# Performance work log

Measured on AMD Instinct MI355X. Metric: run time of the kernel, lower is better.

Reference implementation:

```python
import jax, jax.numpy as jnp
import numpy as np

S, B, L = 64, 32, 64
VS, VT = 32000, 32000
D_EMB, H_ENC, H_DEC = 300, 512, 1024


def _lstm_cell(x, h, c, w_ih, w_hh, b):
    # PyTorch gate order: i, f, g, o
    g = x @ w_ih.T + h @ w_hh.T + b
    i, f, gg, o = jnp.split(g, 4, axis=1)
    c2 = jax.nn.sigmoid(f) * c + jax.nn.sigmoid(i) * jnp.tanh(gg)
    h2 = jax.nn.sigmoid(o) * jnp.tanh(c2)
    return h2, c2


def _lstm_dir(emb, w_ih, w_hh, b, reverse):
    h0 = jnp.zeros((emb.shape[1], H_ENC), emb.dtype)
    def step(carry, x):
        h, c = carry
        h, c = _lstm_cell(x, h, c, w_ih, w_hh, b)
        return (h, c), h
    (hT, cT), ys = jax.lax.scan(step, (h0, h0), emb, reverse=reverse)
    return ys, hT, cT


def setup_inputs() -> dict:
    key = jax.random.key(0)
    ks = jax.random.split(key, 20)
    r = lambda k, shape: (jax.random.normal(k, shape, jnp.float32) * 0.02)
    inp = {
        "eemb": r(ks[0], (VS, D_EMB)),
        "enc_w_ih_f": r(ks[1], (4 * H_ENC, D_EMB)),
        "enc_w_hh_f": r(ks[2], (4 * H_ENC, H_ENC)),
        "enc_b_f": r(ks[3], (4 * H_ENC,)),  # = b_ih + b_hh (summed, identical math)
        "enc_w_ih_b": r(ks[4], (4 * H_ENC, D_EMB)),
        "enc_w_hh_b": r(ks[5], (4 * H_ENC, H_ENC)),
        "enc_b_b": r(ks[6], (4 * H_ENC,)),
        "attn_wi": r(ks[7], (H_DEC, H_DEC)),
        "attn_wo": r(ks[8], (H_DEC, 2 * H_DEC)),
        "dec_w_ih": r(ks[9], (4 * H_DEC, H_DEC + D_EMB)),
        "dec_w_hh": r(ks[10], (4 * H_DEC, H_DEC)),
        "dec_b": r(ks[11], (4 * H_DEC,)),
        "demb": r(ks[12], (VT, D_EMB)),
        "gen_w": r(ks[13], (VT, H_DEC)),
        "gen_b": r(ks[14], (VT,)),
        "input_src_batch": jax.random.randint(ks[15], (S, B), 0, VS),
        "input_trg_batch": jax.random.randint(ks[16], (L, B), 0, VT),
    }
    return inp


def reference(eemb, enc_w_ih_f, enc_w_hh_f, enc_b_f, enc_w_ih_b, enc_w_hh_b,
              enc_b_b, attn_wi, attn_wo, dec_w_ih, dec_w_hh, dec_b, demb,
              gen_w, gen_b, input_src_batch, input_trg_batch):
    emb = eemb[input_src_batch]  # [S,B,300]
    out_f, hf, cf = _lstm_dir(emb, enc_w_ih_f, enc_w_hh_f, enc_b_f, False)
    out_b, hb, cb = _lstm_dir(emb, enc_w_ih_b, enc_w_hh_b, enc_b_b, True)
    enc_out = jnp.concatenate([out_f, out_b], axis=2)  # [S,B,1024]
    bsz = emb.shape[1]
    # permute(1,2,0).view(B,1024): interleave fwd/bwd features
    hidden = jnp.stack([hf, hb], 0).transpose(1, 2, 0).reshape(bsz, H_DEC)
    context = jnp.stack([cf, cb], 0).transpose(1, 2, 0).reshape(bsz, H_DEC)

    trg_emb = demb[input_trg_batch[:-1]]  # [L-1,B,300]

    def dec_step(carry, e):
        h, c = carry
        semi = h @ attn_wi.T  # [B,1024]
        scores = jax.nn.softmax(jnp.sum(enc_out * semi[None], axis=2), axis=0)  # [S,B]
        s_tilde = jnp.sum(scores[:, :, None] * enc_out, axis=0)  # [B,1024]
        c_t = jnp.tanh(jnp.concatenate([s_tilde, h], axis=1) @ attn_wo.T)
        x = jnp.concatenate([c_t, e], axis=1)  # [B,1324]
        h, c = _lstm_cell(x, h, c, dec_w_ih, dec_w_hh, dec_b)
        out = jax.nn.log_softmax(h @ gen_w.T + gen_b, axis=1)  # [B,VT]
        return (h, c), out

    _, ys = jax.lax.scan(dec_step, (hidden, context), trg_emb)  # [L-1,B,VT]
    output = jnp.concatenate([jnp.zeros((1,) + ys.shape[1:], ys.dtype), ys], axis=0)
    return output
```

## Files before the change

kernel.cpp:

```cpp
#include <hip/hip_runtime.h>

typedef __attribute__((ext_vector_type(8))) short short8;
typedef __attribute__((ext_vector_type(4))) float f32x4;
typedef unsigned short u16;
typedef unsigned int u32;

static __device__ __forceinline__ float sigf(float x){ return 1.0f/(1.0f+expf(-x)); }

static __device__ __forceinline__ u16 f2b(float f){
    u32 u = __float_as_uint(f);
    u += 0x7FFFu + ((u>>16)&1u);
    return (u16)(u>>16);
}
static __device__ __forceinline__ float us2f(u16 s){ return __uint_as_float(((u32)s)<<16); }
static __device__ __forceinline__ float b2f_lo(u32 u){ return __uint_as_float(u<<16); }
static __device__ __forceinline__ float b2f_hi(u32 u){ return __uint_as_float(u & 0xffff0000u); }

static __device__ __forceinline__ void st_wt_u16(u16* p, u16 v) {
    asm volatile("global_store_short %0, %1, off sc1" :: "v"(p), "v"((u32)v) : "memory");
}
static __device__ __forceinline__ void st_wt_u32(u32* p, u32 v) {
    asm volatile("global_store_dword %0, %1, off sc1" :: "v"(p), "v"(v) : "memory");
}
static __device__ __forceinline__ u32 ld_cv(const u32* p){
    u32 v;
    asm volatile("global_load_dword %0, %1, off sc0 sc1\ns_waitcnt vmcnt(0)"
                 : "=v"(v) : "v"(p) : "memory");
    return v;
}

static __device__ __forceinline__ void hot_spin() {
    float x = 1.0f;
#pragma unroll
    for (int i = 0; i < 16; ++i) x = __builtin_fmaf(x, 1.0000001f, 1.0e-7f);
    asm volatile("" :: "v"(x));
}

static __device__ __forceinline__ void wait_publish(const u32* base, int n, u32 tgt, u32* rel) {
    if ((int)threadIdx.x < n) {
        const u32* p = base + (size_t)threadIdx.x*32;
        while (ld_cv(p) < tgt) hot_spin();
    }
    __syncthreads();
    if (threadIdx.x == 0) st_wt_u32(rel, tgt);
}
static __device__ __forceinline__ void wait_rel(const u32* rel, u32 tgt) {
    if (threadIdx.x == 0) {
        while (ld_cv(rel) < tgt) hot_spin();
    }
    __syncthreads();
}


__global__ __launch_bounds__(256) void k_zero(float* __restrict__ p, long n) {
    for (long i = (long)blockIdx.x*256 + threadIdx.x; i < n; i += (long)gridDim.x*256) p[i] = 0.0f;
}

__global__ __launch_bounds__(256) void k_wenc(const float* __restrict__ whh, u16* __restrict__ dst) {
    int i = blockIdx.x*256 + threadIdx.x;
    int n = i >> 9, k = i & 511;
    int j = n >> 2, q = n & 3;
    dst[i] = f2b(whh[(size_t)(q*512 + j)*512 + k]);
}

__global__ __launch_bounds__(256) void k_xw(const float* __restrict__ table,
                                            const int* __restrict__ idx,
                                            const float* __restrict__ W,
                                            int wstride, int koff,
                                            const float* __restrict__ bias,
                                            u16* __restrict__ outU, int N,
                                            int jmask, int jshift) {
    __shared__ float Xs[32][300];
    int m0 = blockIdx.y * 32;
    int j0 = blockIdx.x * 64;
    for (int i = threadIdx.x; i < 32*300; i += 256) {
        int r = i/300, c = i - r*300;
        Xs[r][c] = table[(size_t)idx[m0+r]*300 + c];
    }
    __syncthreads();
    int tx = threadIdx.x & 63, ty = threadIdx.x >> 6;
    int jj = j0 + tx;
    const float* wr = W + (size_t)jj*wstride + koff;
    float acc[8] = {0,0,0,0,0,0,0,0};
    for (int k = 0; k < 300; ++k) {
        float w = wr[k];
#pragma unroll
        for (int mi = 0; mi < 8; ++mi) acc[mi] += Xs[ty*8+mi][k] * w;
    }
    float bv = bias[jj];
    int col = ((jj & jmask) << 2) | (jj >> jshift);
#pragma unroll
    for (int mi = 0; mi < 8; ++mi)
        outU[(size_t)(m0 + ty*8 + mi)*N + col] = f2b(acc[mi] + bv);
}

__global__ __launch_bounds__(512, 1) void k_enc(
    const u16* __restrict__ Xf, const u16* __restrict__ Xb,
    const u16* __restrict__ WencB,
    u16* __restrict__ encBX, float* __restrict__ cfin,
    u32* __restrict__ sentE, u32* __restrict__ relE,
    const float* __restrict__ awi, const float* __restrict__ awo,
    const float* __restrict__ dwih, const float* __restrict__ dwhh,
    const float* __restrict__ genw,
    u16* __restrict__ awiTB, u16* __restrict__ awoB,
    u16* __restrict__ WdecB, u16* __restrict__ genw_b)
{
    __shared__ float SH[2304];
    const int tid = threadIdx.x;
    const int bid = blockIdx.x;

    if (bid >= 64) {
        long wid = (long)(bid-64)*512 + tid;
        {
            const float4* s4 = (const float4*)genw;
            ushort4* d4 = (ushort4*)genw_b;
            for (long i = wid; i < 8192000L; i += 98304L) {
                float4 v = s4[i]; ushort4 u;
                u.x=f2b(v.x); u.y=f2b(v.y); u.z=f2b(v.z); u.w=f2b(v.w);
                d4[i]=u;
            }
        }
        for (long i = wid; i < 8388608L; i += 98304L) {
            int n=(int)(i>>11), k=(int)(i&2047);
            int j=n>>2, q=n&3;
            float v=(k<1024)? dwih[(size_t)(q*1024+j)*1324+k]
                            : dwhh[(size_t)(q*1024+j)*1024+(k-1024)];
            WdecB[i]=f2b(v);
        }
        for (long i = wid; i < 1048576L; i += 98304L) {
            int kcol=(int)(i>>10), n=(int)(i&1023);
            awiTB[i]=f2b(awi[(size_t)n*1024+kcol]);
        }
        {
            const float4* s4=(const float4*)awo;
            ushort4* d4=(ushort4*)awoB;
            for (long i = wid; i < 524288L; i += 98304L) {
                float4 v=s4[i]; ushort4 u;
                u.x=f2b(v.x); u.y=f2b(v.y); u.z=f2b(v.z); u.w=f2b(v.w);
                d4[i]=u;
            }
        }
        return;
    }

    const int wv = tid >> 6, lane = tid & 63;
    const int gwave = bid*8 + wv;
    const int lr = lane & 15, lk8 = (lane >> 4)*8;
    const int b_l = lane & 15, jjq = lane >> 4;
    const int g0 = bid & 48;
    u32* relg = relE + (size_t)(g0 >> 4)*32;

    const int dir = gwave >> 8;
    const int mt = (gwave >> 7) & 1;
    const int nt = gwave & 127;
    const int m0 = mt*16, n0 = nt*16;
    const u16* Bw = WencB + (size_t)dir*1048576 + (size_t)(n0+lr)*512 + lk8;
    const u16* Xd = dir ? Xb : Xf;
    float* T = SH + wv*272;
    const int bb = m0 + b_l;
    const int j = nt*4 + jjq;

    short8 bw[16];
#pragma unroll
    for (int i = 0; i < 16; ++i) bw[i] = *(const short8*)(Bw + i*32);

    float creg = 0.f;
    for (int t = 0; t < 64; ++t) {
        if (t > 0) {
            if (bid == g0) wait_publish(sentE + (size_t)g0*32, 16, (u32)t, relg);
            else           wait_rel(relg, (u32)t);
        }
        const int rslot = (t==0) ? 0 : (dir ? (65-t) : t);
        const u16* Ah = encBX + (size_t)rslot*32768 + (size_t)(m0+lr)*1024 + dir*512 + lk8;
        short8 av[16];
#pragma unroll
        for (int i = 0; i < 16; ++i) av[i] = *(const short8*)(Ah + i*32);
        f32x4 acc = {0.f,0.f,0.f,0.f};
#pragma unroll
        for (int i = 0; i < 16; ++i)
            acc = __builtin_amdgcn_mfma_f32_16x16x32_bf16(av[i], bw[i], acc, 0, 0, 0);
        {
            const int rb = (lane>>4)*4;
#pragma unroll
            for (int r = 0; r < 4; ++r) T[(rb+r)*17 + (lane&15)] = acc[r];
        }
        __builtin_amdgcn_sched_barrier(0);
        const int s = dir ? (63-t) : t;
        ushort4 xr = *(const ushort4*)(Xd + (size_t)(s*32+bb)*2048 + n0 + jjq*4);
        float gi = T[b_l*17 + jjq*4 + 0] + us2f(xr.x);
        float gf = T[b_l*17 + jjq*4 + 1] + us2f(xr.y);
        float gg = T[b_l*17 + jjq*4 + 2] + us2f(xr.z);
        float go = T[b_l*17 + jjq*4 + 3] + us2f(xr.w);
        float c2 = sigf(gf)*creg + sigf(gi)*tanhf(gg);
        float h2 = sigf(go)*tanhf(c2);
        creg = c2;
        st_wt_u16(encBX + (size_t)(s+1)*32768 + (size_t)bb*1024 + dir*512 + j, f2b(h2));
        __syncthreads();
        if (tid == 0) st_wt_u32(sentE + (size_t)bid*32, (u32)(t+1));
    }
    cfin[dir*16384 + bb*512 + j] = creg;
}

__global__ __launch_bounds__(256) void k_mid(const u16* __restrict__ encBX,
                                             const u16* __restrict__ awiTB,
                                             const u16* __restrict__ awoB,
                                             u16* __restrict__ encPB,
                                             u16* __restrict__ EOAb,
                                             u16* __restrict__ Hd) {
    if (blockIdx.x < 128) {
        int gt = blockIdx.x*256 + threadIdx.x;
        int b = gt >> 10, jj2 = gt & 1023;
        int d = jj2 & 1, k = jj2 >> 1;
        Hd[(size_t)b*1024 + jj2] = encBX[(size_t)(d ? 1 : 64)*32768 + (size_t)b*1024 + d*512 + k];
        Hd[(size_t)64*32768 + gt] = 0;
    }
    const int wv = threadIdx.x >> 6, lane = threadIdx.x & 63;
    const int lr = lane & 15, lk8 = (lane >> 4)*8;
    const u16* Abase = encBX + 32768;
#pragma unroll
    for (int ii = 0; ii < 4; ++ii) {
        int id = (blockIdx.x*4 + wv)*4 + ii;
        int eoa = id >> 13;
        int id2 = id & 8191;
        int mt2 = id2 >> 6, nt2 = id2 & 63;
        int m0 = mt2*16, n0 = nt2*16;
        const u16* Ar = Abase + (size_t)(m0+lr)*1024 + lk8;
        const u16* Br = eoa ? (awoB + (size_t)(n0+lr)*2048 + lk8)
                            : (awiTB + (size_t)(n0+lr)*1024 + lk8);
        f32x4 acc = {0.f,0.f,0.f,0.f};
#pragma unroll 8
        for (int i = 0; i < 32; ++i) {
            short8 av = *(const short8*)(Ar + i*32);
            short8 bv = *(const short8*)(Br + i*32);
            acc = __builtin_amdgcn_mfma_f32_16x16x32_bf16(av, bv, acc, 0, 0, 0);
        }
        int col = n0 + (lane&15);
        int rb = m0 + (lane>>4)*4;
#pragma unroll
        for (int r = 0; r < 4; ++r) {
            int row = rb + r;
            if (eoa) {
                int b = row & 31, s = row >> 5;
                EOAb[((size_t)b*64 + s)*1024 + col] = f2b(acc[r]);
            } else {
                encPB[(size_t)row*1024 + col] = f2b(acc[r]);
            }
        }
    }
}

__global__ __launch_bounds__(512, 1) void k_dec(
    const u16* __restrict__ Xe,
    const u16* __restrict__ awoB, const u16* __restrict__ WdecB,
    const u16* __restrict__ encPB, const u16* __restrict__ EOAb,
    u16* __restrict__ Hd, u16* __restrict__ PEOb, u16* __restrict__ hAb,
    const float* __restrict__ cfin,
    u32* __restrict__ sentA, u32* __restrict__ sentH,
    u32* __restrict__ relA, u32* __restrict__ relH)
{
    __shared__ float SH[2592];
    __shared__ u32 CT[16512];
    const int tid = threadIdx.x;
    const int bid = blockIdx.x;
    const int wv = tid >> 6, lane = tid & 63;
    const int lr = lane & 15, lk8 = (lane >> 4)*8;
    const int b_l = lane & 15, jjq = lane >> 4;

    const int mt4 = wv & 1, kq4 = wv >> 1;
    const int m0d = mt4*16;
    const int bbd = m0d + b_l;
    const int jd = bid*4 + jjq;
    float cdec = cfin[(jd&1)*16384 + bbd*512 + (jd>>1)];

    short8 wp[16];
#pragma unroll
    for (int i = 0; i < 16; ++i)
        wp[i] = *(const short8*)(WdecB + (size_t)(bid*16+lr)*2048 + kq4*512 + lk8 + i*32);

    const bool isHA = (bid >= 32 && bid < 96);
    const int nth = bid - 32;
    const int mth = wv & 1, kqh = wv >> 1;
    short8 wh[8];
    if (isHA) {
#pragma unroll
        for (int i = 0; i < 8; ++i)
            wh[i] = *(const short8*)(awoB + (size_t)(nth*16+lr)*2048 + 1024 + kqh*256 + lk8 + i*32);
    }

    for (int t = 0; t < 63; ++t) {
        if (bid < 96) {
            if (t > 0) {
                if (bid == 0) wait_publish(sentH, 256, (u32)t, relH);
                else          wait_rel(relH, (u32)t);
            }
            if (bid < 32) {
                const int b = bid;
                float* hsh = SH; float* red = SH + 1024; float* sc = SH + 1536;
                {
                    u32 u = ((const u32*)Hd)[(size_t)t*16384 + b*512 + tid];
                    hsh[2*tid]   = b2f_lo(u);
                    hsh[2*tid+1] = b2f_hi(u);
                }
                __syncthreads();
                {
                    int s = tid >> 3, p = tid & 7;
                    const uint4* ep = (const uint4*)(encPB + (size_t)(s*32+b)*1024 + p*128);
                    const float* hk = hsh + p*128;
                    float a0=0,a1=0,a2=0,a3=0;
#pragma unroll 4
                    for (int q8 = 0; q8 < 16; ++q8) {
                        uint4 u = ep[q8];
                        a0 += b2f_lo(u.x)*hk[q8*8+0] + b2f_hi(u.x)*hk[q8*8+1];
                        a1 += b2f_lo(u.y)*hk[q8*8+2] + b2f_hi(u.y)*hk[q8*8+3];
                        a2 += b2f_lo(u.z)*hk[q8*8+4] + b2f_hi(u.z)*hk[q8*8+5];
                        a3 += b2f_lo(u.w)*hk[q8*8+6] + b2f_hi(u.w)*hk[q8*8+7];
                    }
                    red[tid] = (a0+a1)+(a2+a3);
                }
                __syncthreads();
                if (tid < 64) {
                    float v = 0;
#pragma unroll
                    for (int pp = 0; pp < 8; ++pp) v += red[tid*8+pp];
                    float m = v;
                    for (int off = 32; off; off >>= 1) m = fmaxf(m, __shfl_xor(m, off));
                    float e = expf(v - m);
                    float ss = e;
                    for (int off = 32; off; off >>= 1) ss += __shfl_xor(ss, off);
                    sc[tid] = e / ss;
                }
                __syncthreads();
                {
                    const u32* eo = (const u32*)EOAb + (size_t)b*32768 + tid;
                    float p0 = 0, p1 = 0;
#pragma unroll 8
                    for (int s = 0; s < 64; ++s) {
                        u32 u = eo[(size_t)s*512];
                        float w = sc[s];
                        p0 += w*b2f_lo(u); p1 += w*b2f_hi(u);
                    }
                    u32 pk = (u32)f2b(p0) | ((u32)f2b(p1) << 16);
                    st_wt_u32((u32*)PEOb + (size_t)t*16384 + b*512 + tid, pk);
                }
            } else {
                const u16* Ah = Hd + (size_t)t*32768 + (size_t)(mth*16+lr)*1024 + kqh*256 + lk8;
                short8 av[8];
#pragma unroll
                for (int i = 0; i < 8; ++i) av[i] = *(const short8*)(Ah + i*32);
                f32x4 acc = {0.f,0.f,0.f,0.f};
#pragma unroll
                for (int i = 0; i < 8; ++i)
                    acc = __builtin_amdgcn_mfma_f32_16x16x32_bf16(av[i], wh[i], acc, 0, 0, 0);
#pragma unroll
                for (int r = 0; r < 4; ++r) SH[wv*256 + lane*4 + r] = acc[r];
                __syncthreads();
                if (wv < 2) {
#pragma unroll
                    for (int r = 0; r < 4; ++r) {
                        float sum = SH[(wv+0)*256 + lane*4 + r] + SH[(wv+2)*256 + lane*4 + r]
                                  + SH[(wv+4)*256 + lane*4 + r] + SH[(wv+6)*256 + lane*4 + r];
                        int m = wv*16 + (lane>>4)*4 + r;
                        st_wt_u16(hAb + (size_t)t*32768 + (size_t)m*1024 + nth*16 + (lane&15),
                                  f2b(sum));
                    }
                }
            }
            __syncthreads();
            if (tid == 0) st_wt_u32(sentA + (size_t)bid*32, (u32)(t+1));
        }

        if (bid == 96) wait_publish(sentA, 96, (u32)(t+1), relA);
        else           wait_rel(relA, (u32)(t+1));
        {
            const u32* pe = (const u32*)PEOb + (size_t)t*16384;
            const u32* ha = (const u32*)hAb + (size_t)t*16384;
#pragma unroll
            for (int ii = 0; ii < 32; ++ii) {
                int idx = tid + ii*512;
                u32 up = pe[idx], uh = ha[idx];
                float c0 = tanhf(b2f_lo(up) + b2f_lo(uh));
                float c1 = tanhf(b2f_hi(up) + b2f_hi(uh));
                int b = idx >> 9, nu = idx & 511;
                CT[b*516 + nu] = (u32)f2b(c0) | ((u32)f2b(c1) << 16);
            }
            __syncthreads();

            short8 av[16];
            if (kq4 < 2) {
                const u32* ctrow = CT + (m0d+lr)*516 + kq4*256 + (lk8 >> 1);
#pragma unroll
                for (int i = 0; i < 16; ++i) av[i] = *(const short8*)(ctrow + i*16);
            } else {
                const u16* Ab = Hd + (size_t)t*32768 + (size_t)(m0d+lr)*1024 + (kq4-2)*512 + lk8;
#pragma unroll
                for (int i = 0; i < 16; ++i) av[i] = *(const short8*)(Ab + i*32);
            }
            f32x4 acc = {0.f,0.f,0.f,0.f};
#pragma unroll
            for (int i = 0; i < 16; ++i)
                acc = __builtin_amdgcn_mfma_f32_16x16x32_bf16(av[i], wp[i], acc, 0, 0, 0);
#pragma unroll
            for (int r = 0; r < 4; ++r) SH[wv*256 + lane*4 + r] = acc[r];
            __syncthreads();
            if (wv < 2) {
                float* T = SH + 2048 + wv*272;
#pragma unroll
                for (int r = 0; r < 4; ++r) {
                    float sum = SH[(wv+0)*256 + lane*4 + r] + SH[(wv+2)*256 + lane*4 + r]
                              + SH[(wv+4)*256 + lane*4 + r] + SH[(wv+6)*256 + lane*4 + r];
                    T[((lane>>4)*4 + r)*17 + (lane&15)] = sum;
                }
                __builtin_amdgcn_sched_barrier(0);
                ushort4 xr = *(const ushort4*)(Xe + (size_t)(t*32+bbd)*4096 + bid*16 + jjq*4);
                float gi = T[b_l*17 + jjq*4 + 0] + us2f(xr.x);
                float gf = T[b_l*17 + jjq*4 + 1] + us2f(xr.y);
                float gg = T[b_l*17 + jjq*4 + 2] + us2f(xr.z);
                float go = T[b_l*17 + jjq*4 + 3] + us2f(xr.w);
                float c2 = sigf(gf)*cdec + sigf(gi)*tanhf(gg);
                float h2 = sigf(go)*tanhf(c2);
                cdec = c2;
                st_wt_u16(Hd + (size_t)(t+1)*32768 + (size_t)bbd*1024 + jd, f2b(h2));
            }
            __syncthreads();
            if (tid == 0) st_wt_u32(sentH + (size_t)bid*32, (u32)(t+1));
        }
    }
}

__global__ __launch_bounds__(256) void k_gemm_gen(const short* __restrict__ A,
                                                  const short* __restrict__ B,
                                                  const float* __restrict__ genb,
                                                  float* __restrict__ out) {
    int wave = threadIdx.x >> 6;
    int lane = threadIdx.x & 63;
    int tile = blockIdx.x * 4 + wave;
    int mt = tile & 31;
    int nt = tile >> 5;
    int m0 = mt*64, n0 = nt*64;
    int lr = lane & 15;
    int lk = (lane >> 4)*8;
    f32x4 acc[4][4] = {};
    for (int k0 = 0; k0 < 1024; k0 += 32) {
        short8 a[4], bfr[4];
#pragma unroll
        for (int mi = 0; mi < 4; ++mi)
            a[mi] = *(const short8*)(A + (long)(m0 + mi*16 + lr)*1024 + k0 + lk);
#pragma unroll
        for (int ni = 0; ni < 4; ++ni)
            bfr[ni] = *(const short8*)(B + (long)(n0 + ni*16 + lr)*1024 + k0 + lk);
#pragma unroll
        for (int mi = 0; mi < 4; ++mi)
#pragma unroll
            for (int ni = 0; ni < 4; ++ni)
                acc[mi][ni] = __builtin_amdgcn_mfma_f32_16x16x32_bf16(a[mi], bfr[ni], acc[mi][ni], 0, 0, 0);
    }
    int dcol = lane & 15;
    int drow = (lane >> 4)*4;
#pragma unroll
    for (int mi = 0; mi < 4; ++mi) {
        int mbase = m0 + mi*16 + drow;
#pragma unroll
        for (int ni = 0; ni < 4; ++ni) {
            int n = n0 + ni*16 + dcol;
            float bv = genb[n];
            f32x4 v = acc[mi][ni];
#pragma unroll
            for (int r = 0; r < 4; ++r) {
                int m = mbase + r;
                if (m < 2016) out[(long)(m + 32)*32000 + n] = v[r] + bv;
            }
        }
    }
}

__global__ __launch_bounds__(256) void k_lsm(float* __restrict__ out) {
    long row = 32 + blockIdx.x;
    float* p = out + row*32000L;
    float4* p4 = (float4*)p;
    int tid = threadIdx.x;
    __shared__ float sm[4];
    __shared__ float ss[4];
    float m = -1e30f;
    for (int i = tid; i < 8000; i += 256) {
        float4 v = p4[i];
        m = fmaxf(m, fmaxf(fmaxf(v.x, v.y), fmaxf(v.z, v.w)));
    }
    for (int off = 32; off; off >>= 1) m = fmaxf(m, __shfl_xor(m, off));
    if ((tid & 63) == 0) sm[tid >> 6] = m;
    __syncthreads();
    m = fmaxf(fmaxf(sm[0], sm[1]), fmaxf(sm[2], sm[3]));
    float s = 0;
    for (int i = tid; i < 8000; i += 256) {
        float4 v = p4[i];
        s += expf(v.x - m) + expf(v.y - m) + expf(v.z - m) + expf(v.w - m);
    }
    for (int off = 32; off; off >>= 1) s += __shfl_xor(s, off);
    if ((tid & 63) == 0) ss[tid >> 6] = s;
    __syncthreads();
    s = ss[0] + ss[1] + ss[2] + ss[3];
    float lse = m + logf(s);
    for (int i = tid; i < 8000; i += 256) {
        float4 v = p4[i];
        v.x -= lse; v.y -= lse; v.z -= lse; v.w -= lse;
        p4[i] = v;
    }
}


extern "C" void kernel_launch(void* const* d_in, const int* in_sizes, int n_in,
                              void* d_out, int out_size, void* d_ws, size_t ws_size,
                              hipStream_t stream) {
    const float* eemb  = (const float*)d_in[0];
    const float* ewihf = (const float*)d_in[1];
    const float* ewhhf = (const float*)d_in[2];
    const float* ebf   = (const float*)d_in[3];
    const float* ewihb = (const float*)d_in[4];
    const float* ewhhb = (const float*)d_in[5];
    const float* ebb   = (const float*)d_in[6];
    const float* awi   = (const float*)d_in[7];
    const float* awo   = (const float*)d_in[8];
    const float* dwih  = (const float*)d_in[9];
    const float* dwhh  = (const float*)d_in[10];
    const float* db    = (const float*)d_in[11];
    const float* demb  = (const float*)d_in[12];
    const float* genw  = (const float*)d_in[13];
    const float* genb  = (const float*)d_in[14];
    const int* srci    = (const int*)d_in[15];
    const int* trgi    = (const int*)d_in[16];
    float* out = (float*)d_out;

    float* F = (float*)d_ws;
    u32* S       = (u32*)F;
    u32* sentE   = S;
    u32* sentA   = S + 2048;
    u32* sentH   = S + 5120;
    u32* relE    = S + 13312;
    u32* relA    = S + 13440;
    u32* relH    = S + 13472;
    float* cfin  = F + 16384;
    u16*   U     = (u16*)(F + 49152);

    u16* Xf_    = U;
    u16* Xb_    = U + 4194304u;
    u16* Xe_    = U + 8388608u;
    u16* WencB  = U + 16646144u;
    u16* awiTB  = U + 18743296u;
    u16* awoB   = U + 19791872u;
    u16* WdecB  = U + 21889024u;
    u16* genw_b = U + 30277632u;
    u16* encBX  = U + 63045632u;
    u16* Hd     = U + 65175552u;
    u16* PEOb   = U + 67305472u;
    u16* hAb    = U + 69369856u;
    u16* encPB  = U + 71434240u;
    u16* EOAb   = U + 73531392u;

    k_zero<<<64, 256, 0, stream>>>(F, 16384);
    k_zero<<<64, 256, 0, stream>>>((float*)encBX, 16384);
    k_zero<<<2048, 256, 0, stream>>>(out, 1024000L);

    k_xw<<<dim3(32, 64), 256, 0, stream>>>(eemb, srci, ewihf, 300, 0, ebf, Xf_, 2048, 511, 9);
    k_xw<<<dim3(32, 64), 256, 0, stream>>>(eemb, srci, ewihb, 300, 0, ebb, Xb_, 2048, 511, 9);
    k_xw<<<dim3(64, 63), 256, 0, stream>>>(demb, trgi, dwih, 1324, 1024, db, Xe_, 4096, 1023, 10);

    k_wenc<<<4096, 256, 0, stream>>>(ewhhf, WencB);
    k_wenc<<<4096, 256, 0, stream>>>(ewhhb, WencB + 1048576u);

    k_enc<<<256, 512, 0, stream>>>(Xf_, Xb_, WencB, encBX, cfin, sentE, relE,
                                   awi, awo, dwih, dwhh, genw,
                                   awiTB, awoB, WdecB, genw_b);
    k_mid<<<1024, 256, 0, stream>>>(encBX, awiTB, awoB, encPB, EOAb, Hd);

    k_dec<<<256, 512, 0, stream>>>(Xe_, awoB, WdecB, encPB, EOAb,
                                   Hd, PEOb, hAb, cfin,
                                   sentA, sentH, relA, relH);

    k_gemm_gen<<<4000, 256, 0, stream>>>((const short*)(Hd + 32768u), (const short*)genw_b, genb, out);
    k_lsm<<<2016, 256, 0, stream>>>(out);
}
```

Baseline: 2.995 ms.

## Use fast exp/tanh intrinsics, merge weight conversion, enlarge generator GEMM tiles

Result: faster. 2.633 ms (-12.1%).

```diff
diff --git a/kernel.cpp b/kernel.cpp
--- a/kernel.cpp
+++ b/kernel.cpp
@@ -5,7 +5,11 @@
 typedef unsigned short u16;
 typedef unsigned int u32;
 
-static __device__ __forceinline__ float sigf(float x){ return 1.0f/(1.0f+expf(-x)); }
+static __device__ __forceinline__ float sigf(float x){ return 1.0f/(1.0f+__expf(-x)); }
+static __device__ __forceinline__ float ftanh(float x){
+    float e = __expf(2.0f*x);
+    return 1.0f - 2.0f/(e + 1.0f);
+}
 
 static __device__ __forceinline__ u16 f2b(float f){
     u32 u = __float_as_uint(f);
@@ -56,11 +60,16 @@
     for (long i = (long)blockIdx.x*256 + threadIdx.x; i < n; i += (long)gridDim.x*256) p[i] = 0.0f;
 }
 
-__global__ __launch_bounds__(256) void k_wenc(const float* __restrict__ whh, u16* __restrict__ dst) {
-    int i = blockIdx.x*256 + threadIdx.x;
-    int n = i >> 9, k = i & 511;
+__global__ __launch_bounds__(256) void k_wenc2(const float* __restrict__ whhf,
+                                               const float* __restrict__ whhb,
+                                               u16* __restrict__ dst) {
+    long i = (long)blockIdx.x*256 + threadIdx.x;
+    int half = (int)(i >> 20);
+    int ii = (int)(i & 1048575);
+    int n = ii >> 9, k = ii & 511;
     int j = n >> 2, q = n & 3;
-    dst[i] = f2b(whh[(size_t)(q*512 + j)*512 + k]);
+    const float* w = half ? whhb : whhf;
+    dst[i] = f2b(w[(size_t)(q*512 + j)*512 + k]);
 }
 
 __global__ __launch_bounds__(256) void k_xw(const float* __restrict__ table,
@@ -191,8 +200,8 @@
         float gf = T[b_l*17 + jjq*4 + 1] + us2f(xr.y);
         float gg = T[b_l*17 + jjq*4 + 2] + us2f(xr.z);
         float go = T[b_l*17 + jjq*4 + 3] + us2f(xr.w);
-        float c2 = sigf(gf)*creg + sigf(gi)*tanhf(gg);
-        float h2 = sigf(go)*tanhf(c2);
+        float c2 = sigf(gf)*creg + sigf(gi)*ftanh(gg);
+        float h2 = sigf(go)*ftanh(c2);
         creg = c2;
         st_wt_u16(encBX + (size_t)(s+1)*32768 + (size_t)bb*1024 + dir*512 + j, f2b(h2));
         __syncthreads();
@@ -324,7 +333,7 @@
                     for (int pp = 0; pp < 8; ++pp) v += red[tid*8+pp];
                     float m = v;
                     for (int off = 32; off; off >>= 1) m = fmaxf(m, __shfl_xor(m, off));
-                    float e = expf(v - m);
+                    float e = __expf(v - m);
                     float ss = e;
                     for (int off = 32; off; off >>= 1) ss += __shfl_xor(ss, off);
                     sc[tid] = e / ss;
@@ -378,8 +387,8 @@
             for (int ii = 0; ii < 32; ++ii) {
                 int idx = tid + ii*512;
                 u32 up = pe[idx], uh = ha[idx];
-                float c0 = tanhf(b2f_lo(up) + b2f_lo(uh));
-                float c1 = tanhf(b2f_hi(up) + b2f_hi(uh));
+                float c0 = ftanh(b2f_lo(up) + b2f_lo(uh));
+                float c1 = ftanh(b2f_hi(up) + b2f_hi(uh));
                 int b = idx >> 9, nu = idx & 511;
                 CT[b*516 + nu] = (u32)f2b(c0) | ((u32)f2b(c1) << 16);
             }
@@ -416,8 +425,8 @@
                 float gf = T[b_l*17 + jjq*4 + 1] + us2f(xr.y);
                 float gg = T[b_l*17 + jjq*4 + 2] + us2f(xr.z);
                 float go = T[b_l*17 + jjq*4 + 3] + us2f(xr.w);
-                float c2 = sigf(gf)*cdec + sigf(gi)*tanhf(gg);
-                float h2 = sigf(go)*tanhf(c2);
+                float c2 = sigf(gf)*cdec + sigf(gi)*ftanh(gg);
+                float h2 = sigf(go)*ftanh(c2);
                 cdec = c2;
                 st_wt_u16(Hd + (size_t)(t+1)*32768 + (size_t)bbd*1024 + jd, f2b(h2));
             }
@@ -427,37 +436,36 @@
     }
 }
 
-__global__ __launch_bounds__(256) void k_gemm_gen(const short* __restrict__ A,
-                                                  const short* __restrict__ B,
-                                                  const float* __restrict__ genb,
-                                                  float* __restrict__ out) {
+__global__ __launch_bounds__(256, 1) void k_gemm_gen(const short* __restrict__ A,
+                                                     const short* __restrict__ B,
+                                                     const float* __restrict__ genb,
+                                                     float* __restrict__ out) {
     int wave = threadIdx.x >> 6;
     int lane = threadIdx.x & 63;
     int tile = blockIdx.x * 4 + wave;
-    int mt = tile & 31;
-    int nt = tile >> 5;
-    int m0 = mt*64, n0 = nt*64;
+    int mt = tile & 15;
+    int nt = tile >> 4;
+    int m0 = mt*128, n0 = nt*64;
     int lr = lane & 15;
     int lk = (lane >> 4)*8;
-    f32x4 acc[4][4] = {};
+    f32x4 acc[8][4] = {};
     for (int k0 = 0; k0 < 1024; k0 += 32) {
-        short8 a[4], bfr[4];
-#pragma unroll
-        for (int mi = 0; mi < 4; ++mi)
-            a[mi] = *(const short8*)(A + (long)(m0 + mi*16 + lr)*1024 + k0 + lk);
+        short8 bfr[4];
 #pragma unroll
         for (int ni = 0; ni < 4; ++ni)
             bfr[ni] = *(const short8*)(B + (long)(n0 + ni*16 + lr)*1024 + k0 + lk);
 #pragma unroll
-        for (int mi = 0; mi < 4; ++mi)
+        for (int mi = 0; mi < 8; ++mi) {
+            short8 a = *(const short8*)(A + (long)(m0 + mi*16 + lr)*1024 + k0 + lk);
 #pragma unroll
             for (int ni = 0; ni < 4; ++ni)
-                acc[mi][ni] = __builtin_amdgcn_mfma_f32_16x16x32_bf16(a[mi], bfr[ni], acc[mi][ni], 0, 0, 0);
+                acc[mi][ni] = __builtin_amdgcn_mfma_f32_16x16x32_bf16(a, bfr[ni], acc[mi][ni], 0, 0, 0);
+        }
     }
     int dcol = lane & 15;
     int drow = (lane >> 4)*4;
 #pragma unroll
-    for (int mi = 0; mi < 4; ++mi) {
+    for (int mi = 0; mi < 8; ++mi) {
         int mbase = m0 + mi*16 + drow;
 #pragma unroll
         for (int ni = 0; ni < 4; ++ni) {
@@ -492,13 +500,13 @@
     float s = 0;
     for (int i = tid; i < 8000; i += 256) {
         float4 v = p4[i];
-        s += expf(v.x - m) + expf(v.y - m) + expf(v.z - m) + expf(v.w - m);
+        s += __expf(v.x - m) + __expf(v.y - m) + __expf(v.z - m) + __expf(v.w - m);
     }
     for (int off = 32; off; off >>= 1) s += __shfl_xor(s, off);
     if ((tid & 63) == 0) ss[tid >> 6] = s;
     __syncthreads();
     s = ss[0] + ss[1] + ss[2] + ss[3];
-    float lse = m + logf(s);
+    float lse = m + __logf(s);
     for (int i = tid; i < 8000; i += 256) {
         float4 v = p4[i];
         v.x -= lse; v.y -= lse; v.z -= lse; v.w -= lse;
@@ -563,8 +571,7 @@
     k_xw<<<dim3(32, 64), 256, 0, stream>>>(eemb, srci, ewihb, 300, 0, ebb, Xb_, 2048, 511, 9);
     k_xw<<<dim3(64, 63), 256, 0, stream>>>(demb, trgi, dwih, 1324, 1024, db, Xe_, 4096, 1023, 10);
 
-    k_wenc<<<4096, 256, 0, stream>>>(ewhhf, WencB);
-    k_wenc<<<4096, 256, 0, stream>>>(ewhhb, WencB + 1048576u);
+    k_wenc2<<<8192, 256, 0, stream>>>(ewhhf, ewhhb, WencB);
 
     k_enc<<<256, 512, 0, stream>>>(Xf_, Xb_, WencB, encBX, cfin, sentE, relE,
                                    awi, awo, dwih, dwhh, genw,
@@ -575,6 +582,6 @@
                                    Hd, PEOb, hAb, cfin,
                                    sentA, sentH, relA, relH);
 
-    k_gemm_gen<<<4000, 256, 0, stream>>>((const short*)(Hd + 32768u), (const short*)genw_b, genb, out);
+    k_gemm_gen<<<2000, 256, 0, stream>>>((const short*)(Hd + 32768u), (const short*)genw_b, genb, out);
     k_lsm<<<2016, 256, 0, stream>>>(out);
 }
```
